# Performance work log

Hardware: AMD Instinct MI355X
Metric: run time of the kernel (lower is better)

Reference implementation:

```python
import jax, jax.numpy as jnp
import numpy as np

NUM_GROUPS = 19  # cityscapes classes; groups in the grouped conv
GATES = 4
SLABS = 4  # hidden slabs per class


def setup_inputs() -> dict:
    key = jax.random.key(0)
    k1, k2, k3, k4, k5 = jax.random.split(key, 5)
    B, H, Wd = 4, 256, 512
    x = jax.random.normal(k1, (B, NUM_GROUPS, H, Wd), dtype=jnp.float32)
    h = jax.random.normal(k2, (B, NUM_GROUPS, SLABS, H, Wd), dtype=jnp.float32)
    c = jax.random.normal(k3, (B, NUM_GROUPS, SLABS, H, Wd), dtype=jnp.float32)
    # Conv2d(95 -> 304, k=3, groups=19): weight (304, 5, 3, 3), bias (304,)
    fan_in = 5 * 3 * 3
    bound = 1.0 / np.sqrt(fan_in)
    W = jax.random.uniform(k4, (4 * NUM_GROUPS * SLABS, 5, 3, 3), minval=-bound, maxval=bound, dtype=jnp.float32)
    b = jax.random.uniform(k5, (4 * NUM_GROUPS * SLABS,), minval=-bound, maxval=bound, dtype=jnp.float32)
    return {"x": x, "h": h, "c": c, "W": W, "b": b}


def reference(x, h, c, W, b):
    B, _, H, Wd = x.shape
    # Strided interleave: channel g*5+0 = x[:,g], g*5+1..4 = h[:,g,0..3]
    xh = jnp.concatenate([x[:, :, None], h], axis=2).reshape(B, NUM_GROUPS * 5, H, Wd)
    A = jax.lax.conv_general_dilated(
        xh, W, window_strides=(1, 1), padding=[(1, 1), (1, 1)],
        feature_group_count=NUM_GROUPS,
        dimension_numbers=("NCHW", "OIHW", "NCHW"))
    A = A + b[None, :, None, None]
    A = A.reshape(B, NUM_GROUPS, GATES, SLABS, H, Wd)
    i = jax.nn.sigmoid(A[:, :, 0])
    f = jax.nn.sigmoid(A[:, :, 1])
    o = jax.nn.sigmoid(A[:, :, 2])
    g = jnp.tanh(A[:, :, 3])
    new_c = f * c + i * g
    new_h = o * jnp.tanh(new_c)
    return (new_h, new_c)
```

## Files before the change

kernel.cpp:

```cpp
#include <hip/hip_runtime.h>
#include <hip/hip_bf16.h>

#define NG      19
#define HEIGHT  256
#define WIDTH   512
#define HW      (HEIGHT*WIDTH)
#define BATCH   4
#define TH      16
#define TW      64
#define HALO_R  18
#define HALO_CU 34
#define CH_U32  (HALO_R*HALO_CU)
#define LDS_U32 (5*CH_U32)
#define WFRAG_SHORTS (NG*64*16)
#define BIAS_FLOATS (NG*16)

typedef __attribute__((ext_vector_type(8))) short short8;
typedef __attribute__((ext_vector_type(4))) float f32x4;
typedef __attribute__((ext_vector_type(4))) unsigned int u32x4;

static __device__ __forceinline__ unsigned int bfbits(float f) {
    return (unsigned int)__builtin_bit_cast(unsigned short, __float2bfloat16(f));
}
static __device__ __forceinline__ unsigned int fsh16(unsigned int hi, unsigned int lo) {
    return (unsigned int)((((unsigned long long)hi << 32) | lo) >> 16);
}
__device__ __forceinline__ float fsigmoid(float x) {
    return __builtin_amdgcn_rcpf(1.0f + __builtin_amdgcn_exp2f(-1.44269504f * x));
}
__device__ __forceinline__ float ftanh(float x) {
    return 2.0f * __builtin_amdgcn_rcpf(1.0f + __builtin_amdgcn_exp2f(-2.88539008f * x)) - 1.0f;
}

__global__ void wxform_kernel(const float* __restrict__ W,
                              const float* __restrict__ b,
                              short* __restrict__ wdst,
                              float* __restrict__ bdst) {
    int i = blockIdx.x * 256 + threadIdx.x;
    if (i < WFRAG_SHORTS) {
        int g   = i / 1024;
        int r   = i & 1023;
        int l   = r >> 4;
        int j   = r & 15;
        int q   = l >> 4;
        int row = l & 15;
        int s    = row >> 2;
        int gate = row & 3;
        int half = j >> 3;
        int jj   = j & 7;
        int m  = 8*half + 2*q + (jj >> 2);
        int kc = jj & 3;
        float wv = 0.0f;
        if (m <= 14 && kc < 3) {
            int ic = m / 3, kr = m % 3;
            int oc = g*16 + gate*4 + s;
            wv = W[((oc*5 + ic)*3 + kr)*3 + kc];
        }
        wdst[i] = (short)__builtin_bit_cast(unsigned short, __float2bfloat16(wv));
    } else if (i < WFRAG_SHORTS + BIAS_FLOATS) {
        int idx = i - WFRAG_SHORTS;
        int g = idx >> 4;
        int r = idx & 15;
        int s = r >> 2, gate = r & 3;
        bdst[idx] = b[g*16 + gate*4 + s];
    }
}

__launch_bounds__(256, 4)
__global__ void convlstm_mfma(const float* __restrict__ x,
                              const float* __restrict__ h,
                              const float* __restrict__ c,
                              const short* __restrict__ wfrag,
                              const float* __restrict__ biasp,
                              float* __restrict__ out) {
    __shared__ unsigned int lds[LDS_U32];

    const int t    = threadIdx.x;
    const int bid  = blockIdx.x;
    const int bg   = bid >> 7;
    const int tile = bid & 127;
    const int tr0  = (tile >> 3) * TH;
    const int tc0  = (tile & 7)  * TW;
    const int g    = bg % NG;

    const int w  = t >> 6;
    const int l  = t & 63;
    const int q  = l >> 4;
    const int li = l & 15;

    const int NC_OFF   = BATCH * NG * 4 * HW;
    const int rowbase0 = (bg*4 + q)*HW + (tr0 + w*4)*WIDTH + tc0 + 4*li;
    f32x4 cp[4];
    #pragma unroll
    for (int tr4 = 0; tr4 < 4; ++tr4)
        cp[tr4] = __builtin_nontemporal_load(
            reinterpret_cast<const f32x4*>(c + rowbase0 + tr4*WIDTH));

    const short8* ap = reinterpret_cast<const short8*>(wfrag + (g*64 + l)*16);
    const short8 a_lo = ap[0];
    const short8 a_hi = ap[1];
    f32x4 bias4;
    {
        float4 bv = *reinterpret_cast<const float4*>(biasp + g*16 + q*4);
        bias4[0] = bv.x; bias4[1] = bv.y; bias4[2] = bv.z; bias4[3] = bv.w;
    }

    const float* xb = x + bg * HW;
    const float* hb = h + (bg * 4) * HW;
    for (int p = t; p < LDS_U32; p += 256) {
        int ch  = p / CH_U32;  int rem = p - ch * CH_U32;
        int r   = rem / HALO_CU;
        int j   = rem - r * HALO_CU;
        int gr  = tr0 + r - 1;
        int gc  = tc0 + 2*j - 1;
        const float* base = (ch == 0) ? xb : hb + (ch - 1) * HW;
        float v0 = 0.0f, v1 = 0.0f;
        if (gr >= 0 && gr < HEIGHT) {
            const float* rowp = base + gr * WIDTH;
            if (gc >= 0 && gc < WIDTH) v0 = rowp[gc];
            if (gc + 1 < WIDTH)        v1 = rowp[gc + 1];
        }
        lds[p] = bfbits(v0) | (bfbits(v1) << 16);
    }
    __syncthreads();

    int cbase[4];
    #pragma unroll
    for (int i = 0; i < 4; ++i) {
        int m = (i < 2) ? (2*q + i) : (8 + 2*q + (i - 2));
        if (m > 14) m = 14;
        cbase[i] = (m/3)*(CH_U32*4) + (m%3)*(HALO_CU*4) + 8*li;
    }
    const char* ldsb = reinterpret_cast<const char*>(lds);

    #pragma unroll
    for (int tr4 = 0; tr4 < 4; ++tr4) {
        const int tr = w*4 + tr4;
        uint2 dv[4][2];
        #pragma unroll
        for (int i = 0; i < 4; ++i) {
            const uint2* pp = reinterpret_cast<const uint2*>(
                ldsb + cbase[i] + tr * (HALO_CU*4));
            dv[i][0] = pp[0];
            dv[i][1] = pp[1];
        }
        float nh4[4], nc4[4];
        #pragma unroll
        for (int n = 0; n < 4; ++n) {
            u32x4 blo_u, bhi_u;
            #pragma unroll
            for (int i = 0; i < 4; ++i) {
                const unsigned int d0 = dv[i][0].x, d1 = dv[i][0].y;
                const unsigned int d2 = dv[i][1].x, d3 = dv[i][1].y;
                unsigned int w0, w1;
                if (n == 0)      { w0 = d0;           w1 = d1;           }
                else if (n == 1) { w0 = fsh16(d1,d0); w1 = fsh16(d2,d1); }
                else if (n == 2) { w0 = d1;           w1 = d2;           }
                else             { w0 = fsh16(d2,d1); w1 = fsh16(d3,d2); }
                if (i < 2) { blo_u[2*i]     = w0; blo_u[2*i+1]     = w1; }
                else       { bhi_u[2*(i-2)] = w0; bhi_u[2*(i-2)+1] = w1; }
            }
            const short8 blo = __builtin_bit_cast(short8, blo_u);
            const short8 bhi = __builtin_bit_cast(short8, bhi_u);

            f32x4 acc = bias4;
            acc = __builtin_amdgcn_mfma_f32_16x16x32_bf16(a_lo, blo, acc, 0, 0, 0);
            acc = __builtin_amdgcn_mfma_f32_16x16x32_bf16(a_hi, bhi, acc, 0, 0, 0);

            const float cv = cp[tr4][n];
            const float iv = fsigmoid(acc[0]);
            const float fv = fsigmoid(acc[1]);
            const float ov = fsigmoid(acc[2]);
            const float gv = ftanh   (acc[3]);
            const float nc = fv * cv + iv * gv;
            nc4[n] = nc;
            nh4[n] = ov * ftanh(nc);
        }
        const int rowchan = rowbase0 + tr4*WIDTH;
        f32x4 nhv; nhv[0]=nh4[0]; nhv[1]=nh4[1]; nhv[2]=nh4[2]; nhv[3]=nh4[3];
        f32x4 ncv; ncv[0]=nc4[0]; ncv[1]=nc4[1]; ncv[2]=nc4[2]; ncv[3]=nc4[3];
        __builtin_nontemporal_store(nhv, reinterpret_cast<f32x4*>(out + rowchan));
        __builtin_nontemporal_store(ncv, reinterpret_cast<f32x4*>(out + NC_OFF + rowchan));
    }
}

extern "C" void kernel_launch(void* const* d_in, const int* in_sizes, int n_in,
                              void* d_out, int out_size, void* d_ws, size_t ws_size,
                              hipStream_t stream) {
    (void)in_sizes; (void)n_in; (void)out_size; (void)ws_size;
    const float* x = (const float*)d_in[0];
    const float* h = (const float*)d_in[1];
    const float* c = (const float*)d_in[2];
    const float* W = (const float*)d_in[3];
    const float* b = (const float*)d_in[4];
    float* out = (float*)d_out;

    short* wdst = (short*)d_ws;
    float* bdst = (float*)((char*)d_ws + WFRAG_SHORTS * sizeof(short));

    hipLaunchKernelGGL(wxform_kernel,
                       dim3((WFRAG_SHORTS + BIAS_FLOATS + 255) / 256), dim3(256),
                       0, stream, W, b, wdst, bdst);
    hipLaunchKernelGGL(convlstm_mfma, dim3(BATCH * NG * 128), dim3(256),
                       0, stream, x, h, c, (const short*)wdst, bdst, out);
}
```

Baseline: 146.5 us.

## Make blocks persistent over four column tiles with register-prefetched halo staging

Each block now handles four consecutive 64-wide column tiles in a loop and cuts the grid by four. The next tile's halo is prefetched into registers as 8-byte vector loads with precomputed offsets and masks, then written to LDS between barriers so global latency overlaps compute. The halo origin moves to an even column so loads align, and the B-fragment shift pattern changes to match. The log2e and sign scaling for the gate activations is folded into the transformed weights and bias, saving multiplies. The risks are fewer blocks to hide latency, more registers, and extra barriers per tile.

```diff
diff --git a/kernel.cpp b/kernel.cpp
--- a/kernel.cpp
+++ b/kernel.cpp
@@ -7,28 +7,34 @@
 #define HW      (HEIGHT*WIDTH)
 #define BATCH   4
 #define TH      16
-#define TW      64
+#define NT      4
 #define HALO_R  18
 #define HALO_CU 34
 #define CH_U32  (HALO_R*HALO_CU)
 #define LDS_U32 (5*CH_U32)
+#define STAGE_TOT LDS_U32
+#define STAGE_PER 12
 #define WFRAG_SHORTS (NG*64*16)
 #define BIAS_FLOATS (NG*16)
 
 typedef __attribute__((ext_vector_type(8))) short short8;
 typedef __attribute__((ext_vector_type(4))) float f32x4;
+typedef __attribute__((ext_vector_type(2))) float f32x2;
 typedef __attribute__((ext_vector_type(4))) unsigned int u32x4;
 
 static __device__ __forceinline__ unsigned int bfbits(float f) {
     return (unsigned int)__builtin_bit_cast(unsigned short, __float2bfloat16(f));
 }
+static __device__ __forceinline__ unsigned int pack2(float lo, float hi) {
+    return bfbits(lo) | (bfbits(hi) << 16);
+}
 static __device__ __forceinline__ unsigned int fsh16(unsigned int hi, unsigned int lo) {
     return (unsigned int)((((unsigned long long)hi << 32) | lo) >> 16);
 }
-__device__ __forceinline__ float fsigmoid(float x) {
-    return __builtin_amdgcn_rcpf(1.0f + __builtin_amdgcn_exp2f(-1.44269504f * x));
-}
-__device__ __forceinline__ float ftanh(float x) {
+static __device__ __forceinline__ float sig2(float a) {
+    return __builtin_amdgcn_rcpf(1.0f + __builtin_amdgcn_exp2f(a));
+}
+static __device__ __forceinline__ float ftanh(float x) {
     return 2.0f * __builtin_amdgcn_rcpf(1.0f + __builtin_amdgcn_exp2f(-2.88539008f * x)) - 1.0f;
 }
 
@@ -54,7 +60,8 @@
         if (m <= 14 && kc < 3) {
             int ic = m / 3, kr = m % 3;
             int oc = g*16 + gate*4 + s;
-            wv = W[((oc*5 + ic)*3 + kr)*3 + kc];
+            float scale = (gate == 3) ? -2.88539008f : -1.44269504f;
+            wv = scale * W[((oc*5 + ic)*3 + kr)*3 + kc];
         }
         wdst[i] = (short)__builtin_bit_cast(unsigned short, __float2bfloat16(wv));
     } else if (i < WFRAG_SHORTS + BIAS_FLOATS) {
@@ -62,7 +69,8 @@
         int g = idx >> 4;
         int r = idx & 15;
         int s = r >> 2, gate = r & 3;
-        bdst[idx] = b[g*16 + gate*4 + s];
+        float scale = (gate == 3) ? -2.88539008f : -1.44269504f;
+        bdst[idx] = scale * b[g*16 + gate*4 + s];
     }
 }
 
@@ -75,26 +83,18 @@
                               float* __restrict__ out) {
     __shared__ unsigned int lds[LDS_U32];
 
-    const int t    = threadIdx.x;
-    const int bid  = blockIdx.x;
-    const int bg   = bid >> 7;
-    const int tile = bid & 127;
-    const int tr0  = (tile >> 3) * TH;
-    const int tc0  = (tile & 7)  * TW;
-    const int g    = bg % NG;
+    const int t     = threadIdx.x;
+    const int bid   = blockIdx.x;
+    const int plane = bid >> 5;
+    const int rem   = bid & 31;
+    const int tr0   = (rem >> 1) * TH;
+    const int tcb   = (rem & 1) * 256;
+    const int g     = plane % NG;
 
     const int w  = t >> 6;
     const int l  = t & 63;
     const int q  = l >> 4;
     const int li = l & 15;
-
-    const int NC_OFF   = BATCH * NG * 4 * HW;
-    const int rowbase0 = (bg*4 + q)*HW + (tr0 + w*4)*WIDTH + tc0 + 4*li;
-    f32x4 cp[4];
-    #pragma unroll
-    for (int tr4 = 0; tr4 < 4; ++tr4)
-        cp[tr4] = __builtin_nontemporal_load(
-            reinterpret_cast<const f32x4*>(c + rowbase0 + tr4*WIDTH));
 
     const short8* ap = reinterpret_cast<const short8*>(wfrag + (g*64 + l)*16);
     const short8 a_lo = ap[0];
@@ -105,24 +105,28 @@
         bias4[0] = bv.x; bias4[1] = bv.y; bias4[2] = bv.z; bias4[3] = bv.w;
     }
 
-    const float* xb = x + bg * HW;
-    const float* hb = h + (bg * 4) * HW;
-    for (int p = t; p < LDS_U32; p += 256) {
-        int ch  = p / CH_U32;  int rem = p - ch * CH_U32;
-        int r   = rem / HALO_CU;
-        int j   = rem - r * HALO_CU;
-        int gr  = tr0 + r - 1;
-        int gc  = tc0 + 2*j - 1;
-        const float* base = (ch == 0) ? xb : hb + (ch - 1) * HW;
-        float v0 = 0.0f, v1 = 0.0f;
-        if (gr >= 0 && gr < HEIGHT) {
-            const float* rowp = base + gr * WIDTH;
-            if (gc >= 0 && gc < WIDTH) v0 = rowp[gc];
-            if (gc + 1 < WIDTH)        v1 = rowp[gc + 1];
-        }
-        lds[p] = bfbits(v0) | (bfbits(v1) << 16);
-    }
-    __syncthreads();
+    const float* xb = x + plane * HW;
+    const float* hb = h + (plane * 4) * HW;
+    int soff[STAGE_PER];
+    int meta[STAGE_PER];
+    #pragma unroll
+    for (int k = 0; k < STAGE_PER; ++k) {
+        int p  = t + 256*k;
+        int v  = (p < STAGE_TOT) ? 1 : 0;
+        int pp = v ? p : 0;
+        int ch = pp / CH_U32;
+        int r2 = pp - ch*CH_U32;
+        int r  = r2 / HALO_CU;
+        int j2 = r2 - r*HALO_CU;
+        int gr = tr0 + r - 1;
+        int rok = ((unsigned)gr < HEIGHT) ? 1 : 0;
+        int isx = (ch == 0) ? 1 : 0;
+        soff[k] = (isx ? 0 : (ch-1)*HW) + gr*WIDTH + 2*j2 - 2;
+        meta[k] = (ch*CH_U32 + r*HALO_CU + j2)
+                | (v << 16) | (rok << 17)
+                | ((j2 == 0) ? (1<<18) : 0) | ((j2 == 33) ? (1<<19) : 0)
+                | (isx << 20);
+    }
 
     int cbase[4];
     #pragma unroll
@@ -132,55 +136,109 @@
         cbase[i] = (m/3)*(CH_U32*4) + (m%3)*(HALO_CU*4) + 8*li;
     }
     const char* ldsb = reinterpret_cast<const char*>(lds);
-
-    #pragma unroll
-    for (int tr4 = 0; tr4 < 4; ++tr4) {
-        const int tr = w*4 + tr4;
-        uint2 dv[4][2];
-        #pragma unroll
-        for (int i = 0; i < 4; ++i) {
-            const uint2* pp = reinterpret_cast<const uint2*>(
-                ldsb + cbase[i] + tr * (HALO_CU*4));
-            dv[i][0] = pp[0];
-            dv[i][1] = pp[1];
-        }
-        float nh4[4], nc4[4];
-        #pragma unroll
-        for (int n = 0; n < 4; ++n) {
-            u32x4 blo_u, bhi_u;
+    const int NC_OFF = BATCH * NG * 4 * HW;
+
+    f32x2 pf[STAGE_PER];
+
+    auto stage_issue = [&](int tc0) {
+        const bool lt = (tc0 == 0), rt = (tc0 == 448);
+        #pragma unroll
+        for (int k = 0; k < STAGE_PER; ++k) {
+            const int mk = meta[k];
+            bool ok = (mk & (1<<16)) && (mk & (1<<17))
+                   && !(lt && (mk & (1<<18))) && !(rt && (mk & (1<<19)));
+            const float* bp = (mk & (1<<20)) ? xb : hb;
+            f32x2 z; z[0] = 0.0f; z[1] = 0.0f;
+            pf[k] = ok ? *reinterpret_cast<const f32x2*>(bp + soff[k] + tc0) : z;
+        }
+    };
+    auto stage_write = [&]() {
+        #pragma unroll
+        for (int k = 0; k < STAGE_PER; ++k) {
+            const int mk = meta[k];
+            if (mk & (1<<16))
+                lds[mk & 0xFFFF] = pack2(pf[k][0], pf[k][1]);
+        }
+    };
+
+    stage_issue(tcb);
+    stage_write();
+    stage_issue(tcb + 64);
+    asm volatile("s_waitcnt lgkmcnt(0)" ::: "memory");
+    __builtin_amdgcn_s_barrier();
+    asm volatile("" ::: "memory");
+
+    #pragma unroll 1
+    for (int tt = 0; tt < NT; ++tt) {
+        const int tc0 = tcb + 64*tt;
+        const int rowbase0 = (plane*4 + q)*HW + (tr0 + w*4)*WIDTH + tc0 + 4*li;
+
+        f32x4 cp[4];
+        #pragma unroll
+        for (int tr4 = 0; tr4 < 4; ++tr4)
+            cp[tr4] = __builtin_nontemporal_load(
+                reinterpret_cast<const f32x4*>(c + rowbase0 + tr4*WIDTH));
+
+        #pragma unroll
+        for (int tr4 = 0; tr4 < 4; ++tr4) {
+            const int tr = w*4 + tr4;
+            uint2 dv[4][2];
             #pragma unroll
             for (int i = 0; i < 4; ++i) {
-                const unsigned int d0 = dv[i][0].x, d1 = dv[i][0].y;
-                const unsigned int d2 = dv[i][1].x, d3 = dv[i][1].y;
-                unsigned int w0, w1;
-                if (n == 0)      { w0 = d0;           w1 = d1;           }
-                else if (n == 1) { w0 = fsh16(d1,d0); w1 = fsh16(d2,d1); }
-                else if (n == 2) { w0 = d1;           w1 = d2;           }
-                else             { w0 = fsh16(d2,d1); w1 = fsh16(d3,d2); }
-                if (i < 2) { blo_u[2*i]     = w0; blo_u[2*i+1]     = w1; }
-                else       { bhi_u[2*(i-2)] = w0; bhi_u[2*(i-2)+1] = w1; }
+                const uint2* pp2 = reinterpret_cast<const uint2*>(
+                    ldsb + cbase[i] + tr*(HALO_CU*4));
+                dv[i][0] = pp2[0];
+                dv[i][1] = pp2[1];
             }
-            const short8 blo = __builtin_bit_cast(short8, blo_u);
-            const short8 bhi = __builtin_bit_cast(short8, bhi_u);
-
-            f32x4 acc = bias4;
-            acc = __builtin_amdgcn_mfma_f32_16x16x32_bf16(a_lo, blo, acc, 0, 0, 0);
-            acc = __builtin_amdgcn_mfma_f32_16x16x32_bf16(a_hi, bhi, acc, 0, 0, 0);
-
-            const float cv = cp[tr4][n];
-            const float iv = fsigmoid(acc[0]);
-            const float fv = fsigmoid(acc[1]);
-            const float ov = fsigmoid(acc[2]);
-            const float gv = ftanh   (acc[3]);
-            const float nc = fv * cv + iv * gv;
-            nc4[n] = nc;
-            nh4[n] = ov * ftanh(nc);
-        }
-        const int rowchan = rowbase0 + tr4*WIDTH;
-        f32x4 nhv; nhv[0]=nh4[0]; nhv[1]=nh4[1]; nhv[2]=nh4[2]; nhv[3]=nh4[3];
-        f32x4 ncv; ncv[0]=nc4[0]; ncv[1]=nc4[1]; ncv[2]=nc4[2]; ncv[3]=nc4[3];
-        __builtin_nontemporal_store(nhv, reinterpret_cast<f32x4*>(out + rowchan));
-        __builtin_nontemporal_store(ncv, reinterpret_cast<f32x4*>(out + NC_OFF + rowchan));
+            float nh4[4], nc4[4];
+            #pragma unroll
+            for (int n = 0; n < 4; ++n) {
+                u32x4 blo_u, bhi_u;
+                #pragma unroll
+                for (int i = 0; i < 4; ++i) {
+                    const unsigned d0 = dv[i][0].x, d1 = dv[i][0].y;
+                    const unsigned d2 = dv[i][1].x, d3 = dv[i][1].y;
+                    unsigned w0, w1;
+                    if (n == 0)      { w0 = fsh16(d1,d0); w1 = fsh16(d2,d1); }
+                    else if (n == 1) { w0 = d1;           w1 = d2;           }
+                    else if (n == 2) { w0 = fsh16(d2,d1); w1 = fsh16(d3,d2); }
+                    else             { w0 = d2;           w1 = d3;           }
+                    if (i < 2) { blo_u[2*i]     = w0; blo_u[2*i+1]     = w1; }
+                    else       { bhi_u[2*(i-2)] = w0; bhi_u[2*(i-2)+1] = w1; }
+                }
+                const short8 blo = __builtin_bit_cast(short8, blo_u);
+                const short8 bhi = __builtin_bit_cast(short8, bhi_u);
+
+                f32x4 acc = bias4;
+                acc = __builtin_amdgcn_mfma_f32_16x16x32_bf16(a_lo, blo, acc, 0, 0, 0);
+                acc = __builtin_amdgcn_mfma_f32_16x16x32_bf16(a_hi, bhi, acc, 0, 0, 0);
+
+                const float cv = cp[tr4][n];
+                const float iv = sig2(acc[0]);
+                const float fv = sig2(acc[1]);
+                const float ov = sig2(acc[2]);
+                const float gv = 2.0f * sig2(acc[3]) - 1.0f;
+                const float nc = fv * cv + iv * gv;
+                nc4[n] = nc;
+                nh4[n] = ov * ftanh(nc);
+            }
+            const int rowchan = rowbase0 + tr4*WIDTH;
+            f32x4 nhv; nhv[0]=nh4[0]; nhv[1]=nh4[1]; nhv[2]=nh4[2]; nhv[3]=nh4[3];
+            f32x4 ncv; ncv[0]=nc4[0]; ncv[1]=nc4[1]; ncv[2]=nc4[2]; ncv[3]=nc4[3];
+            __builtin_nontemporal_store(nhv, reinterpret_cast<f32x4*>(out + rowchan));
+            __builtin_nontemporal_store(ncv, reinterpret_cast<f32x4*>(out + NC_OFF + rowchan));
+        }
+
+        if (tt + 1 < NT) {
+            asm volatile("" ::: "memory");
+            __builtin_amdgcn_s_barrier();
+            asm volatile("" ::: "memory");
+            stage_write();
+            if (tt + 2 < NT) stage_issue(tcb + 64*(tt + 2));
+            asm volatile("s_waitcnt lgkmcnt(0)" ::: "memory");
+            __builtin_amdgcn_s_barrier();
+            asm volatile("" ::: "memory");
+        }
     }
 }
 
@@ -201,6 +259,6 @@
     hipLaunchKernelGGL(wxform_kernel,
                        dim3((WFRAG_SHORTS + BIAS_FLOATS + 255) / 256), dim3(256),
                        0, stream, W, b, wdst, bdst);
-    hipLaunchKernelGGL(convlstm_mfma, dim3(BATCH * NG * 128), dim3(256),
+    hipLaunchKernelGGL(convlstm_mfma, dim3(BATCH * NG * 32), dim3(256),
                        0, stream, x, h, c, (const short*)wdst, bdst, out);
 }
```

New measurement: 144.0 us. Within noise of the previous version (-1.7%).
